# Kernel optimization log

Measured on AMD Instinct MI355X. Metric: run time of the kernel, lower is better.

Reference implementation:

```python
import jax, jax.numpy as jnp
import numpy as np

F_DIM, C_DIM, L_DIM, H_DIM = 28, 10, 28, 100  # feature, class, latent, hidden
LEVEL = 4
CODEBOOK = jnp.array([0.25, 0.3536, 0.5, 0.7071, 1.0, 1.4142, 2.0, 2.8284, 4.0], dtype=jnp.float32)


def setup_inputs() -> dict:
    key = jax.random.key(0)
    ks = jax.random.split(key, 20)
    w = lambda k, shape: (jax.random.normal(k, shape, jnp.float32) * 0.1)
    return {
        "x": jax.random.uniform(ks[0], (F_DIM,), jnp.float32),
        "y": jax.random.uniform(ks[1], (C_DIM,), jnp.float32),
        "eps": jax.random.normal(ks[2], (LEVEL, L_DIM), jnp.float32),
        # fc1: (feature+class) -> 100
        "W1": w(ks[3], (H_DIM, F_DIM + C_DIM)), "b1": w(ks[4], (H_DIM,)),
        # fc2_mu / fc2_log_std: 100 -> latent
        "W2m": w(ks[5], (L_DIM, H_DIM)), "b2m": w(ks[6], (L_DIM,)),
        "W2s": w(ks[7], (L_DIM, H_DIM)), "b2s": w(ks[8], (L_DIM,)),
        # fc3: (latent+class) -> 100
        "W3": w(ks[9], (H_DIM, L_DIM + C_DIM)), "b3": w(ks[10], (H_DIM,)),
        # fc4: 100 -> feature
        "W4": w(ks[11], (F_DIM, H_DIM)), "b4": w(ks[12], (F_DIM,)),
        # fc5: latent -> 100, fc6_mu: 100 -> latent
        "W5": w(ks[13], (H_DIM, L_DIM)), "b5": w(ks[14], (H_DIM,)),
        "W6": w(ks[15], (L_DIM, H_DIM)), "b6": w(ks[16], (L_DIM,)),
    }


def reference(x, y, eps, W1, b1, W2m, b2m, W2s, b2s, W3, b3, W4, b4, W5, b5, W6, b6):
    def enc(v):
        h = jax.nn.relu(W1 @ jnp.concatenate([v, y]) + b1)
        return W2m @ h + b2m, jax.nn.sigmoid(W2s @ h + b2s)

    def dec(z):
        h = jax.nn.relu(W3 @ jnp.concatenate([z, y]) + b3)
        return jax.nn.sigmoid(W4 @ h + b4)

    def quant(z):
        # vectorized nearest-codebook: |z_j - c_i| argmin over 9 codes
        idx = jnp.argmin(jnp.abs(z[:, None] - CODEBOOK[None, :]), axis=1)
        return CODEBOOK[idx]

    def mu_dec(r):
        return W6 @ (W5 @ r + b5) + b6  # fc6_mu(fc5(r)), no activation

    mu0, ls0 = enc(x)
    d1 = quant(mu0 + eps[0] * ls0)
    mu1, ls1 = enc(d1)
    d2 = quant(mu1 + eps[1] * ls1)
    mu2, ls2 = enc(d2)
    d3 = quant(mu2 + eps[2] * ls2)
    mu3, ls3 = enc(d3)
    d4 = quant(mu3 + eps[3] * ls3)

    recon3 = dec(d4); mud3 = mu_dec(recon3)
    recon2 = dec(quant(recon3)); mud2 = mu_dec(recon2)
    recon1 = dec(quant(recon2)); mud1 = mu_dec(recon1)
    recon0 = dec(quant(recon1)); mud0 = mu_dec(recon0)

    zeros = jnp.zeros((L_DIM,), dtype=x.dtype)
    mu_e = jnp.stack([mu0, mu1, mu2, zeros])       # row 3 never written in torch code
    logstd = jnp.stack([ls0, ls1, ls2, zeros])
    mu_d = jnp.stack([mud0, mud1, mud2, mud3])
    return recon0, mu_e, mu_d, logstd
```

## Files before the change

### kernel.cpp

```cpp
#include <hip/hip_runtime.h>
#include <math.h>

#define NT 256

__device__ __forceinline__ float sigmoid_f(float v) {
    return 1.0f / (1.0f + expf(-v));
}

__device__ __forceinline__ float quant_f(float z) {
    float best = 0.25f;
    float bd = fabsf(z - 0.25f);
    const float cbs[8] = {0.3536f, 0.5f, 0.7071f, 1.0f, 1.4142f, 2.0f, 2.8284f, 4.0f};
#pragma unroll
    for (int i = 0; i < 8; i++) {
        float d = fabsf(z - cbs[i]);
        if (d < bd) { bd = d; best = cbs[i]; }
    }
    return best;
}

template<int N4>
__device__ __forceinline__ float dot_rl(const float* wr, const float* v) {
    const float4* v4 = (const float4*)v;
    float a0 = 0.f, a1 = 0.f, a2 = 0.f, a3 = 0.f;
#pragma unroll
    for (int i = 0; i < N4; i++) {
        float4 vv = v4[i];
        a0 = fmaf(wr[4*i+0], vv.x, a0);
        a1 = fmaf(wr[4*i+1], vv.y, a1);
        a2 = fmaf(wr[4*i+2], vv.z, a2);
        a3 = fmaf(wr[4*i+3], vv.w, a3);
    }
    return (a0 + a1) + (a2 + a3);
}

__device__ __forceinline__ int sliceStart(int g) {
    return g == 0 ? 0 : (g == 1 ? 28 : (g == 2 ? 52 : 76));
}

__global__ __launch_bounds__(NT, 1) void cvae_kernel(
    const float* __restrict__ x, const float* __restrict__ y, const float* __restrict__ eps,
    const float* __restrict__ W1, const float* __restrict__ b1,
    const float* __restrict__ W2m, const float* __restrict__ b2m,
    const float* __restrict__ W2s, const float* __restrict__ b2s,
    const float* __restrict__ W3, const float* __restrict__ b3,
    const float* __restrict__ W4, const float* __restrict__ b4,
    const float* __restrict__ W5, const float* __restrict__ b5,
    const float* __restrict__ W6, const float* __restrict__ b6,
    float* __restrict__ out)
{
    const int tid = threadIdx.x;

    __shared__ __align__(16) float cat0[20];
    __shared__ __align__(16) float cat1[20];
    __shared__ __align__(16) float cat2v[40];
    __shared__ __align__(16) float h_lds[4][28];
    __shared__ __align__(16) float t_lds[4][28];
    __shared__ __align__(16) float rec_lds[2][16];

    const int r1 = tid >> 1, p1 = tid & 1;
    const int r2 = tid >> 3, c2 = tid & 7;
    const int g2 = c2 & 3;
    const int r4 = tid >> 2, g4 = tid & 3;
    const int r3 = tid - 128;

    const int hg  = (r1 < 28) ? 0 : ((r1 < 52) ? 1 : ((r1 < 76) ? 2 : 3));
    const int ho  = hg * 28 + (r1 - sliceStart(hg));
    const int h3g = (r3 < 28) ? 0 : ((r3 < 52) ? 1 : ((r3 < 76) ? 2 : 3));
    const int h3o = h3g * 28 + (r3 - sliceStart(h3g));

    float w1s[20]; float b1r = 0.f;
    if (tid < 200) {
        const float2* s2 = (const float2*)(W1 + r1 * 38 + p1 * 20);
        if (p1 == 0) {
#pragma unroll
            for (int i = 0; i < 10; i++) { float2 v = s2[i]; w1s[2*i] = v.x; w1s[2*i+1] = v.y; }
            b1r = b1[r1];
        } else {
#pragma unroll
            for (int i = 0; i < 9; i++) { float2 v = s2[i]; w1s[2*i] = v.x; w1s[2*i+1] = v.y; }
            w1s[18] = 0.f; w1s[19] = 0.f;
        }
    }

    float w2s[28]; float b2r = 0.f; float er[4] = {0.f, 0.f, 0.f, 0.f};
    if (tid < 224) {
        const float* mat = (c2 < 4) ? W2m : W2s;
        const float4* s4 = (const float4*)(mat + r2 * 100 + sliceStart(g2));
        if (g2 == 0) {
#pragma unroll
            for (int i = 0; i < 7; i++) { float4 v = s4[i]; w2s[4*i] = v.x; w2s[4*i+1] = v.y; w2s[4*i+2] = v.z; w2s[4*i+3] = v.w; }
        } else {
#pragma unroll
            for (int i = 0; i < 6; i++) { float4 v = s4[i]; w2s[4*i] = v.x; w2s[4*i+1] = v.y; w2s[4*i+2] = v.z; w2s[4*i+3] = v.w; }
            w2s[24] = 0.f; w2s[25] = 0.f; w2s[26] = 0.f; w2s[27] = 0.f;
        }
        if (c2 == 0) {
            b2r = b2m[r2];
            er[0] = eps[r2]; er[1] = eps[28 + r2]; er[2] = eps[56 + r2]; er[3] = eps[84 + r2];
        }
        if (c2 == 4) b2r = b2s[r2];
    }

    float w4s[28], w6s[28]; float b4r = 0.f, b6r = 0.f;
    if (tid < 112) {
        const float4* s4 = (const float4*)(W4 + r4 * 100 + sliceStart(g4));
        const float4* s6 = (const float4*)(W6 + r4 * 100 + sliceStart(g4));
        if (g4 == 0) {
#pragma unroll
            for (int i = 0; i < 7; i++) { float4 v = s4[i]; w4s[4*i] = v.x; w4s[4*i+1] = v.y; w4s[4*i+2] = v.z; w4s[4*i+3] = v.w; }
#pragma unroll
            for (int i = 0; i < 7; i++) { float4 v = s6[i]; w6s[4*i] = v.x; w6s[4*i+1] = v.y; w6s[4*i+2] = v.z; w6s[4*i+3] = v.w; }
            b4r = b4[r4]; b6r = b6[r4];
        } else {
#pragma unroll
            for (int i = 0; i < 6; i++) { float4 v = s4[i]; w4s[4*i] = v.x; w4s[4*i+1] = v.y; w4s[4*i+2] = v.z; w4s[4*i+3] = v.w; }
#pragma unroll
            for (int i = 0; i < 6; i++) { float4 v = s6[i]; w6s[4*i] = v.x; w6s[4*i+1] = v.y; w6s[4*i+2] = v.z; w6s[4*i+3] = v.w; }
            w4s[24] = 0.f; w4s[25] = 0.f; w4s[26] = 0.f; w4s[27] = 0.f;
            w6s[24] = 0.f; w6s[25] = 0.f; w6s[26] = 0.f; w6s[27] = 0.f;
        }
    }

    float w5s[16]; float b5r = 0.f;
    if (tid < 200) {
        const float2* s2 = (const float2*)(W5 + r1 * 28 + p1 * 14);
#pragma unroll
        for (int i = 0; i < 7; i++) { float2 v = s2[i]; w5s[2*i] = v.x; w5s[2*i+1] = v.y; }
        w5s[14] = 0.f; w5s[15] = 0.f;
        if (p1 == 0) b5r = b5[r1];
    }

    float w3s[40]; float b3r = 0.f;
    if (tid >= 128 && tid < 228) {
        const float2* s2 = (const float2*)(W3 + r3 * 38);
#pragma unroll
        for (int i = 0; i < 19; i++) { float2 v = s2[i]; w3s[2*i] = v.x; w3s[2*i+1] = v.y; }
        w3s[38] = 0.f; w3s[39] = 0.f;
        b3r = b3[r3];
    }

    if (tid < 28) {
        float xv = x[tid];
        if (tid < 20) cat0[tid] = xv; else cat1[tid - 20] = xv;
        out[112 + tid] = 0.f;
        out[336 + tid] = 0.f;
    }
    if (tid < 10) { float yv = y[tid]; cat1[8 + tid] = yv; cat2v[28 + tid] = yv; }
    if (tid == 0) { cat1[18] = 0.f; cat1[19] = 0.f; cat2v[38] = 0.f; cat2v[39] = 0.f; }
    if (tid >= 1 && tid < 4) {
#pragma unroll
        for (int j = 24; j < 28; j++) { h_lds[tid][j] = 0.f; t_lds[tid][j] = 0.f; }
    }
    if (tid < 2) { rec_lds[tid][14] = 0.f; rec_lds[tid][15] = 0.f; }
    __syncthreads();

#pragma unroll
    for (int lev = 0; lev < 4; lev++) {
        if (tid < 200) {
            float s = dot_rl<5>(w1s, p1 ? cat1 : cat0);
            s += __shfl_xor(s, 1);
            if (p1 == 0) ((float*)h_lds)[ho] = fmaxf(s + b1r, 0.f);
        }
        __syncthreads();

        if (tid < 224) {
            float s = dot_rl<7>(w2s, h_lds[g2]);
            s += __shfl_xor(s, 1);
            s += __shfl_xor(s, 2);
            float fin = 0.f;
            if (c2 == 0)      fin = s + b2r;
            else if (c2 == 4) fin = sigmoid_f(s + b2r);
            float oth = __shfl_xor(fin, 4);
            if (c2 == 0) {
                float z = quant_f(fmaf(er[lev], oth, fin));
                if (r2 < 20) cat0[r2] = z; else cat1[r2 - 20] = z;
                cat2v[r2] = z;
                if (lev < 3) out[28 + lev * 28 + r2] = fin;
            } else if (c2 == 4 && lev < 3) {
                out[252 + lev * 28 + r2] = fin;
            }
        }
        __syncthreads();
    }

    if (tid >= 128 && tid < 228) {
        float s = dot_rl<10>(w3s, cat2v);
        ((float*)h_lds)[h3o] = fmaxf(s + b3r, 0.f);
    }
    __syncthreads();

    for (int s3 = 3; s3 >= 0; s3--) {
        if (tid < 112) {
            float s = dot_rl<7>(w4s, h_lds[g4]);
            s += __shfl_xor(s, 1);
            s += __shfl_xor(s, 2);
            if (g4 == 0) {
                float rv = sigmoid_f(s + b4r);
                if (r4 < 14) rec_lds[0][r4] = rv; else rec_lds[1][r4 - 14] = rv;
                cat2v[r4] = quant_f(rv);
                if (s3 == 0) out[r4] = rv;
            }
        }
        __syncthreads();

        if (tid < 200) {
            float s = dot_rl<4>(w5s, p1 ? rec_lds[1] : rec_lds[0]);
            s += __shfl_xor(s, 1);
            if (p1 == 0) ((float*)t_lds)[ho] = s + b5r;
        }
        __syncthreads();

        if (tid < 112) {
            float s = dot_rl<7>(w6s, t_lds[g4]);
            s += __shfl_xor(s, 1);
            s += __shfl_xor(s, 2);
            if (g4 == 0) out[140 + s3 * 28 + r4] = s + b6r;
        } else if (s3 > 0 && tid >= 128 && tid < 228) {
            float s = dot_rl<10>(w3s, cat2v);
            ((float*)h_lds)[h3o] = fmaxf(s + b3r, 0.f);
        }
        __syncthreads();
    }
}

extern "C" void kernel_launch(void* const* d_in, const int* in_sizes, int n_in,
                              void* d_out, int out_size, void* d_ws, size_t ws_size,
                              hipStream_t stream) {
    const float* x   = (const float*)d_in[0];
    const float* y   = (const float*)d_in[1];
    const float* eps = (const float*)d_in[2];
    const float* W1  = (const float*)d_in[3];
    const float* b1  = (const float*)d_in[4];
    const float* W2m = (const float*)d_in[5];
    const float* b2m = (const float*)d_in[6];
    const float* W2s = (const float*)d_in[7];
    const float* b2s = (const float*)d_in[8];
    const float* W3  = (const float*)d_in[9];
    const float* b3  = (const float*)d_in[10];
    const float* W4  = (const float*)d_in[11];
    const float* b4  = (const float*)d_in[12];
    const float* W5  = (const float*)d_in[13];
    const float* b5  = (const float*)d_in[14];
    const float* W6  = (const float*)d_in[15];
    const float* b6  = (const float*)d_in[16];
    float* out = (float*)d_out;

    cvae_kernel<<<1, NT, 0, stream>>>(x, y, eps, W1, b1, W2m, b2m, W2s, b2s,
                                      W3, b3, W4, b4, W5, b5, W6, b6, out);
}
```

Baseline: 16.29 us.

## Defer mu_dec off the decoder critical path and batch outputs through LDS

The fc5/fc6 mu_dec work moves out of the serial four-step decoder chain. The chain now runs only fc4 and fc3 per step and stores each reconstruction. After the loop, all four mu_dec evaluations run at once: fc5 processes two reconstructions per thread, and fc6 splits each row into two halves across 224 threads. All outputs are staged in a shared buffer and written with a single float4 copy at the end, which removes scattered global stores and two barriers per decoder step. The cost is more registers per thread (52-wide W6 slice, 28-wide W5 row) and extra shared memory.

```diff
diff --git a/kernel.cpp b/kernel.cpp
--- a/kernel.cpp
+++ b/kernel.cpp
@@ -55,14 +55,19 @@
     __shared__ __align__(16) float cat1[20];
     __shared__ __align__(16) float cat2v[40];
     __shared__ __align__(16) float h_lds[4][28];
-    __shared__ __align__(16) float t_lds[4][28];
-    __shared__ __align__(16) float rec_lds[2][16];
+    __shared__ __align__(16) float rec4[4][32];
+    __shared__ __align__(16) float t_b[4][112];
+    __shared__ __align__(16) float ostash[364];
 
     const int r1 = tid >> 1, p1 = tid & 1;
     const int r2 = tid >> 3, c2 = tid & 7;
     const int g2 = c2 & 3;
     const int r4 = tid >> 2, g4 = tid & 3;
     const int r3 = tid - 128;
+    const int s3lo = (tid >= 100) ? 1 : 0;
+    const int j5 = tid - 100 * s3lo;
+    const int idx6 = tid >> 1, p6 = tid & 1;
+    const int s36 = idx6 / 28, i6 = idx6 - 28 * s36;
 
     const int hg  = (r1 < 28) ? 0 : ((r1 < 52) ? 1 : ((r1 < 76) ? 2 : 3));
     const int ho  = hg * 28 + (r1 - sliceStart(hg));
@@ -102,33 +107,40 @@
         if (c2 == 4) b2r = b2s[r2];
     }
 
-    float w4s[28], w6s[28]; float b4r = 0.f, b6r = 0.f;
+    float w4s[28]; float b4r = 0.f;
     if (tid < 112) {
         const float4* s4 = (const float4*)(W4 + r4 * 100 + sliceStart(g4));
-        const float4* s6 = (const float4*)(W6 + r4 * 100 + sliceStart(g4));
         if (g4 == 0) {
 #pragma unroll
             for (int i = 0; i < 7; i++) { float4 v = s4[i]; w4s[4*i] = v.x; w4s[4*i+1] = v.y; w4s[4*i+2] = v.z; w4s[4*i+3] = v.w; }
-#pragma unroll
-            for (int i = 0; i < 7; i++) { float4 v = s6[i]; w6s[4*i] = v.x; w6s[4*i+1] = v.y; w6s[4*i+2] = v.z; w6s[4*i+3] = v.w; }
-            b4r = b4[r4]; b6r = b6[r4];
+            b4r = b4[r4];
         } else {
 #pragma unroll
             for (int i = 0; i < 6; i++) { float4 v = s4[i]; w4s[4*i] = v.x; w4s[4*i+1] = v.y; w4s[4*i+2] = v.z; w4s[4*i+3] = v.w; }
-#pragma unroll
-            for (int i = 0; i < 6; i++) { float4 v = s6[i]; w6s[4*i] = v.x; w6s[4*i+1] = v.y; w6s[4*i+2] = v.z; w6s[4*i+3] = v.w; }
             w4s[24] = 0.f; w4s[25] = 0.f; w4s[26] = 0.f; w4s[27] = 0.f;
-            w6s[24] = 0.f; w6s[25] = 0.f; w6s[26] = 0.f; w6s[27] = 0.f;
-        }
-    }
-
-    float w5s[16]; float b5r = 0.f;
+        }
+    }
+
+    float w5f[28]; float b5r = 0.f;
     if (tid < 200) {
-        const float2* s2 = (const float2*)(W5 + r1 * 28 + p1 * 14);
-#pragma unroll
-        for (int i = 0; i < 7; i++) { float2 v = s2[i]; w5s[2*i] = v.x; w5s[2*i+1] = v.y; }
-        w5s[14] = 0.f; w5s[15] = 0.f;
-        if (p1 == 0) b5r = b5[r1];
+        const float4* s4 = (const float4*)(W5 + j5 * 28);
+#pragma unroll
+        for (int i = 0; i < 7; i++) { float4 v = s4[i]; w5f[4*i] = v.x; w5f[4*i+1] = v.y; w5f[4*i+2] = v.z; w5f[4*i+3] = v.w; }
+        b5r = b5[j5];
+    }
+
+    float w6h[52]; float b6r = 0.f;
+    if (tid < 224) {
+        const float4* s4 = (const float4*)(W6 + i6 * 100 + 52 * p6);
+        if (p6 == 0) {
+#pragma unroll
+            for (int i = 0; i < 13; i++) { float4 v = s4[i]; w6h[4*i] = v.x; w6h[4*i+1] = v.y; w6h[4*i+2] = v.z; w6h[4*i+3] = v.w; }
+            b6r = b6[i6];
+        } else {
+#pragma unroll
+            for (int i = 0; i < 12; i++) { float4 v = s4[i]; w6h[4*i] = v.x; w6h[4*i+1] = v.y; w6h[4*i+2] = v.z; w6h[4*i+3] = v.w; }
+            w6h[48] = 0.f; w6h[49] = 0.f; w6h[50] = 0.f; w6h[51] = 0.f;
+        }
     }
 
     float w3s[40]; float b3r = 0.f;
@@ -143,16 +155,19 @@
     if (tid < 28) {
         float xv = x[tid];
         if (tid < 20) cat0[tid] = xv; else cat1[tid - 20] = xv;
-        out[112 + tid] = 0.f;
-        out[336 + tid] = 0.f;
+        ostash[112 + tid] = 0.f;
+        ostash[336 + tid] = 0.f;
     }
     if (tid < 10) { float yv = y[tid]; cat1[8 + tid] = yv; cat2v[28 + tid] = yv; }
     if (tid == 0) { cat1[18] = 0.f; cat1[19] = 0.f; cat2v[38] = 0.f; cat2v[39] = 0.f; }
     if (tid >= 1 && tid < 4) {
 #pragma unroll
-        for (int j = 24; j < 28; j++) { h_lds[tid][j] = 0.f; t_lds[tid][j] = 0.f; }
-    }
-    if (tid < 2) { rec_lds[tid][14] = 0.f; rec_lds[tid][15] = 0.f; }
+        for (int j = 24; j < 28; j++) h_lds[tid][j] = 0.f;
+    }
+    if (tid >= 32 && tid < 96) {
+        int r = (tid - 32) >> 4, c = 96 + ((tid - 32) & 15);
+        t_b[r][c] = 0.f;
+    }
     __syncthreads();
 
 #pragma unroll
@@ -176,9 +191,9 @@
                 float z = quant_f(fmaf(er[lev], oth, fin));
                 if (r2 < 20) cat0[r2] = z; else cat1[r2 - 20] = z;
                 cat2v[r2] = z;
-                if (lev < 3) out[28 + lev * 28 + r2] = fin;
+                if (lev < 3) ostash[28 + lev * 28 + r2] = fin;
             } else if (c2 == 4 && lev < 3) {
-                out[252 + lev * 28 + r2] = fin;
+                ostash[252 + lev * 28 + r2] = fin;
             }
         }
         __syncthreads();
@@ -197,31 +212,38 @@
             s += __shfl_xor(s, 2);
             if (g4 == 0) {
                 float rv = sigmoid_f(s + b4r);
-                if (r4 < 14) rec_lds[0][r4] = rv; else rec_lds[1][r4 - 14] = rv;
+                rec4[s3][r4] = rv;
                 cat2v[r4] = quant_f(rv);
-                if (s3 == 0) out[r4] = rv;
+                if (s3 == 0) ostash[r4] = rv;
             }
         }
         __syncthreads();
 
-        if (tid < 200) {
-            float s = dot_rl<4>(w5s, p1 ? rec_lds[1] : rec_lds[0]);
-            s += __shfl_xor(s, 1);
-            if (p1 == 0) ((float*)t_lds)[ho] = s + b5r;
-        }
-        __syncthreads();
-
-        if (tid < 112) {
-            float s = dot_rl<7>(w6s, t_lds[g4]);
-            s += __shfl_xor(s, 1);
-            s += __shfl_xor(s, 2);
-            if (g4 == 0) out[140 + s3 * 28 + r4] = s + b6r;
-        } else if (s3 > 0 && tid >= 128 && tid < 228) {
-            float s = dot_rl<10>(w3s, cat2v);
-            ((float*)h_lds)[h3o] = fmaxf(s + b3r, 0.f);
-        }
-        __syncthreads();
-    }
+        if (s3 > 0) {
+            if (tid >= 128 && tid < 228) {
+                float s = dot_rl<10>(w3s, cat2v);
+                ((float*)h_lds)[h3o] = fmaxf(s + b3r, 0.f);
+            }
+            __syncthreads();
+        }
+    }
+
+    if (tid < 200) {
+        float sA = dot_rl<7>(w5f, rec4[s3lo]);
+        float sB = dot_rl<7>(w5f, rec4[s3lo + 2]);
+        t_b[s3lo][j5]     = sA + b5r;
+        t_b[s3lo + 2][j5] = sB + b5r;
+    }
+    __syncthreads();
+
+    if (tid < 224) {
+        float s = dot_rl<13>(w6h, &t_b[s36][52 * p6]);
+        s += __shfl_xor(s, 1);
+        if (p6 == 0) ostash[140 + s36 * 28 + i6] = s + b6r;
+    }
+    __syncthreads();
+
+    if (tid < 91) ((float4*)out)[tid] = ((const float4*)ostash)[tid];
 }
 
 extern "C" void kernel_launch(void* const* d_in, const int* in_sizes, int n_in,
```

New measurement: 16.39 us. No clear change (+0.6%).
